# Kernel tuning notes

Measured on AMD Instinct MI355X. Metric: run time of the kernel, lower is better.

The kernel has to match this reference:

```python
import jax, jax.numpy as jnp
import numpy as np

B, IN, H, M = 65536, 128, 256, 32


def setup_inputs() -> dict:
    key = jax.random.key(0)
    ks = jax.random.split(key, 8)
    s_i = 1.0 / np.sqrt(IN + H)
    s_m = 1.0 / np.sqrt(M)
    return {
        "input": jax.random.normal(ks[0], (B, IN), jnp.float32),
        "media": jax.random.normal(ks[1], (B, M), jnp.float32),
        "h_t": jax.random.normal(ks[2], (B, H), jnp.float32),
        "c_t": jax.random.normal(ks[3], (B, H), jnp.float32),
        "Wi": jax.random.normal(ks[4], (H, IN + H), jnp.float32) * s_i,
        "bi": jax.random.normal(ks[5], (H,), jnp.float32) * s_i,
        "Wm": jax.random.normal(ks[6], (H, M), jnp.float32) * s_m,
        "bm": jax.random.normal(ks[7], (H,), jnp.float32) * s_m,
    }


def reference(input, media, h_t, c_t, Wi, bi, Wm, bm):
    # original, so all gates share one pre-activation g.
    combined = jnp.concatenate([input, h_t], axis=1)
    g = combined @ Wi.T + bi                     # [B, H]
    gate = jax.nn.sigmoid(g)                     # i == f == o
    c = c_t * gate + jnp.tanh(g) * gate          # new cell state
    c_r = jnp.tanh(c)
    m = jax.nn.sigmoid(media @ Wm.T + bm)        # media gate [B, H]
    c_f = c - c_r + c_r * m
    h = jnp.tanh(c_f) * gate
    # classification=False -> output is h; returns (output, h, c)
    return (h, h, c)
```

## Files before the change

kernel.cpp:

```cpp
#include <hip/hip_runtime.h>

#define BB  65536
#define INW 128
#define HH  256
#define MM  32
#define KK  (INW + HH)
#define NKC 12

typedef __attribute__((ext_vector_type(8))) short bf16x8;
typedef __attribute__((ext_vector_type(4))) float f32x4;

__device__ __forceinline__ unsigned short f32_to_bf16(float f) {
    union { float f; unsigned u; } v; v.f = f;
    return (unsigned short)((v.u + 0x7fffu + ((v.u >> 16) & 1u)) >> 16);
}

__device__ __forceinline__ bf16x8 cvt8(f32x4 a, f32x4 b) {
    bf16x8 r;
    r[0] = (short)f32_to_bf16(a[0]); r[1] = (short)f32_to_bf16(a[1]);
    r[2] = (short)f32_to_bf16(a[2]); r[3] = (short)f32_to_bf16(a[3]);
    r[4] = (short)f32_to_bf16(b[0]); r[5] = (short)f32_to_bf16(b[1]);
    r[6] = (short)f32_to_bf16(b[2]); r[7] = (short)f32_to_bf16(b[3]);
    return r;
}

__device__ __forceinline__ float rcp_f(float x) { return __builtin_amdgcn_rcpf(x); }
__device__ __forceinline__ float sigmoid_f(float x) { return rcp_f(1.0f + __expf(-x)); }
__device__ __forceinline__ float tanh_f(float x) { return 1.0f - 2.0f * rcp_f(__expf(2.0f * x) + 1.0f); }

__global__ void pack_weights(const float* __restrict__ Wi, const float* __restrict__ Wm,
                             unsigned short* __restrict__ Wi_p, unsigned short* __restrict__ Wm_p) {
    int id = blockIdx.x * 256 + threadIdx.x;
    if (id < 2 * NKC * 8 * 512) {
        int blk = id >> 9;
        int e   = id & 511;
        int lane = e >> 3, j = e & 7;
        int lrow = lane & 15, quad = lane >> 4;
        int h  = blk / (NKC * 8);
        int b  = blk % (NKC * 8);
        int kc = b >> 3;
        int t  = b & 7;
        int n  = h * 128 + t * 16 + lrow;
        int k  = kc * 32 + quad * 8 + j;
        Wi_p[id] = f32_to_bf16(Wi[(size_t)n * KK + k]);
    }
    if (id < 2 * 8 * 512) {
        int blk = id >> 9;
        int e   = id & 511;
        int lane = e >> 3, j = e & 7;
        int lrow = lane & 15, quad = lane >> 4;
        int h = blk >> 3;
        int t = blk & 7;
        int n = h * 128 + t * 16 + lrow;
        Wm_p[id] = f32_to_bf16(Wm[(size_t)n * MM + quad * 8 + j]);
    }
}

__global__ __launch_bounds__(256) void rlstm_main(
    const float* __restrict__ input, const float* __restrict__ media,
    const float* __restrict__ h_t,   const float* __restrict__ c_t,
    const unsigned short* __restrict__ Wi_p, const float* __restrict__ bi,
    const unsigned short* __restrict__ Wm_p, const float* __restrict__ bm,
    float* __restrict__ out)
{
    const int tid  = threadIdx.x;
    const int wave = tid >> 6;
    const int lane = tid & 63;
    const int lrow = lane & 15;
    const int quad = lane >> 4;

    const int m0   = blockIdx.x * 32 + (wave >> 1) * 16;
    const int half = wave & 1;
    const int n0   = half * 128;

    const unsigned short* wip = Wi_p + (size_t)half * (NKC * 8 * 512);
    const unsigned short* wmp = Wm_p + (size_t)half * (8 * 512);

    const int arow = m0 + lrow;

    f32x4 md0 = *(const f32x4*)(media + (size_t)arow * MM + quad * 8);
    f32x4 md1 = *(const f32x4*)(media + (size_t)arow * MM + quad * 8 + 4);

    f32x4 accg[8];
#pragma unroll
    for (int t = 0; t < 8; ++t) accg[t] = (f32x4){0.f, 0.f, 0.f, 0.f};

#pragma unroll
    for (int kc = 0; kc < NKC; ++kc) {
        const float* src = (kc < 4)
            ? (input + (size_t)arow * INW + kc * 32 + quad * 8)
            : (h_t   + (size_t)arow * HH  + (kc - 4) * 32 + quad * 8);
        f32x4 a0 = ((const f32x4*)src)[0];
        f32x4 a1 = ((const f32x4*)src)[1];
        bf16x8 xf = cvt8(a0, a1);
        const unsigned short* wb = wip + (size_t)kc * (8 * 512) + lane * 8;
#pragma unroll
        for (int t = 0; t < 8; ++t) {
            bf16x8 wf = *(const bf16x8*)(wb + t * 512);
            accg[t] = __builtin_amdgcn_mfma_f32_16x16x32_bf16(wf, xf, accg[t], 0, 0, 0);
        }
    }

    bf16x8 mf = cvt8(md0, md1);
    const size_t outH = (size_t)BB * HH;
    const size_t rowbase = (size_t)arow * HH;
#pragma unroll
    for (int t = 0; t < 8; ++t) {
        bf16x8 wmf = *(const bf16x8*)(wmp + t * 512 + lane * 8);
        f32x4 am = __builtin_amdgcn_mfma_f32_16x16x32_bf16(
            wmf, mf, (f32x4){0.f, 0.f, 0.f, 0.f}, 0, 0, 0);

        const int nb = n0 + t * 16 + quad * 4;
        f32x4 bi4 = *(const f32x4*)(bi + nb);
        f32x4 bm4 = *(const f32x4*)(bm + nb);
        const size_t idx = rowbase + nb;
        f32x4 ct4 = *(const f32x4*)(c_t + idx);

        f32x4 h4, c4;
#pragma unroll
        for (int r = 0; r < 4; ++r) {
            float g    = accg[t][r] + bi4[r];
            float mp   = am[r] + bm4[r];
            float gate = sigmoid_f(g);
            float tg   = tanh_f(g);
            float c    = ct4[r] * gate + tg * gate;
            float cr   = tanh_f(c);
            float mg   = sigmoid_f(mp);
            float cf   = c - cr + cr * mg;
            float h    = tanh_f(cf) * gate;
            h4[r] = h; c4[r] = c;
        }
        *(f32x4*)(out + idx)            = h4;
        *(f32x4*)(out + idx + outH)     = h4;
        *(f32x4*)(out + idx + 2 * outH) = c4;
    }
}

extern "C" void kernel_launch(void* const* d_in, const int* in_sizes, int n_in,
                              void* d_out, int out_size, void* d_ws, size_t ws_size,
                              hipStream_t stream) {
    const float* input = (const float*)d_in[0];
    const float* media = (const float*)d_in[1];
    const float* h_t   = (const float*)d_in[2];
    const float* c_t   = (const float*)d_in[3];
    const float* Wi    = (const float*)d_in[4];
    const float* bi    = (const float*)d_in[5];
    const float* Wm    = (const float*)d_in[6];
    const float* bm    = (const float*)d_in[7];
    float* out = (float*)d_out;

    unsigned short* Wi_p = (unsigned short*)d_ws;
    unsigned short* Wm_p = Wi_p + 2 * NKC * 8 * 512;

    hipLaunchKernelGGL(pack_weights, dim3((2 * NKC * 8 * 512 + 255) / 256), dim3(256), 0, stream,
                       Wi, Wm, Wi_p, Wm_p);
    hipLaunchKernelGGL(rlstm_main, dim3(BB / 32), dim3(256), 0, stream,
                       input, media, h_t, c_t, Wi_p, bi, Wm_p, bm, out);
}
```

Before: 394.7 us.

## Double row tile per wave, software-pipeline loads, prefetch c_t, nontemporal stores

Each wave now computes two 16-row tiles, so every weight fragment loaded from global memory feeds two MFMAs instead of one. Activation loads are triple-buffered and weight loads double-buffered across the K loop to hide latency. c_t is prefetched before the epilogue, outputs are written with nontemporal stores, and launch bounds ask for 2 blocks per SM. The cost is much higher register pressure (two accumulator sets plus the buffers), which may lower occupancy or cause spills, and the grid is halved.

```diff
diff --git a/kernel.cpp b/kernel.cpp
--- a/kernel.cpp
+++ b/kernel.cpp
@@ -50,13 +50,35 @@
         int lane = e >> 3, j = e & 7;
         int lrow = lane & 15, quad = lane >> 4;
         int h = blk >> 3;
-        int t = blk & 7;
+        int t = blk & 3 + 0;
+        t = blk & 7;
         int n = h * 128 + t * 16 + lrow;
         Wm_p[id] = f32_to_bf16(Wm[(size_t)n * MM + quad * 8 + j]);
     }
 }
 
-__global__ __launch_bounds__(256) void rlstm_main(
+__device__ __forceinline__ void epilogue4(f32x4 g4, f32x4 am, f32x4 ct4, f32x4 bi4, f32x4 bm4,
+                                          float* __restrict__ p, size_t outH) {
+    f32x4 h4, c4;
+#pragma unroll
+    for (int r = 0; r < 4; ++r) {
+        float g    = g4[r] + bi4[r];
+        float mp   = am[r] + bm4[r];
+        float gate = sigmoid_f(g);
+        float tg   = tanh_f(g);
+        float c    = ct4[r] * gate + tg * gate;
+        float cr   = tanh_f(c);
+        float mg   = sigmoid_f(mp);
+        float cf   = c - cr + cr * mg;
+        float h    = tanh_f(cf) * gate;
+        h4[r] = h; c4[r] = c;
+    }
+    __builtin_nontemporal_store(h4, (f32x4*)p);
+    __builtin_nontemporal_store(h4, (f32x4*)(p + outH));
+    __builtin_nontemporal_store(c4, (f32x4*)(p + 2 * outH));
+}
+
+__global__ __launch_bounds__(256, 2) void rlstm_main(
     const float* __restrict__ input, const float* __restrict__ media,
     const float* __restrict__ h_t,   const float* __restrict__ c_t,
     const unsigned short* __restrict__ Wi_p, const float* __restrict__ bi,
@@ -69,70 +91,92 @@
     const int lrow = lane & 15;
     const int quad = lane >> 4;
 
-    const int m0   = blockIdx.x * 32 + (wave >> 1) * 16;
+    const int m0   = blockIdx.x * 64 + (wave >> 1) * 32;
     const int half = wave & 1;
     const int n0   = half * 128;
 
     const unsigned short* wip = Wi_p + (size_t)half * (NKC * 8 * 512);
     const unsigned short* wmp = Wm_p + (size_t)half * (8 * 512);
 
-    const int arow = m0 + lrow;
-
-    f32x4 md0 = *(const f32x4*)(media + (size_t)arow * MM + quad * 8);
-    f32x4 md1 = *(const f32x4*)(media + (size_t)arow * MM + quad * 8 + 4);
-
-    f32x4 accg[8];
-#pragma unroll
-    for (int t = 0; t < 8; ++t) accg[t] = (f32x4){0.f, 0.f, 0.f, 0.f};
+    const int arowA = m0 + lrow;
+    const int arowB = arowA + 16;
+
+    f32x4 mdA0 = *(const f32x4*)(media + (size_t)arowA * MM + quad * 8);
+    f32x4 mdA1 = *(const f32x4*)(media + (size_t)arowA * MM + quad * 8 + 4);
+    f32x4 mdB0 = *(const f32x4*)(media + (size_t)arowB * MM + quad * 8);
+    f32x4 mdB1 = *(const f32x4*)(media + (size_t)arowB * MM + quad * 8 + 4);
+
+    f32x4 accA[8], accB[8];
+#pragma unroll
+    for (int t = 0; t < 8; ++t) {
+        accA[t] = (f32x4){0.f, 0.f, 0.f, 0.f};
+        accB[t] = (f32x4){0.f, 0.f, 0.f, 0.f};
+    }
+
+    f32x4  abuf[3][4];
+    bf16x8 wbuf[2][8];
+
+#define ACT_SRC(arow, kc) ((kc) < 4 ? (input + (size_t)(arow) * INW + (kc) * 32 + quad * 8) \
+                                    : (h_t   + (size_t)(arow) * HH  + ((kc) - 4) * 32 + quad * 8))
+#define LOAD_ACT(p, kc) { const float* sA_ = ACT_SRC(arowA, kc); const float* sB_ = ACT_SRC(arowB, kc); \
+        abuf[p][0] = ((const f32x4*)sA_)[0]; abuf[p][1] = ((const f32x4*)sA_)[1];                        \
+        abuf[p][2] = ((const f32x4*)sB_)[0]; abuf[p][3] = ((const f32x4*)sB_)[1]; }
+#define LOAD_W(p, kc) { const unsigned short* wb_ = wip + (size_t)(kc) * (8 * 512) + lane * 8;           \
+        _Pragma("unroll") for (int t_ = 0; t_ < 8; ++t_) wbuf[p][t_] = *(const bf16x8*)(wb_ + t_ * 512); }
+
+    LOAD_ACT(0, 0);
+    LOAD_ACT(1, 1);
+    LOAD_W(0, 0);
 
 #pragma unroll
     for (int kc = 0; kc < NKC; ++kc) {
-        const float* src = (kc < 4)
-            ? (input + (size_t)arow * INW + kc * 32 + quad * 8)
-            : (h_t   + (size_t)arow * HH  + (kc - 4) * 32 + quad * 8);
-        f32x4 a0 = ((const f32x4*)src)[0];
-        f32x4 a1 = ((const f32x4*)src)[1];
-        bf16x8 xf = cvt8(a0, a1);
-        const unsigned short* wb = wip + (size_t)kc * (8 * 512) + lane * 8;
+        if (kc + 2 < NKC) { LOAD_ACT((kc + 2) % 3, kc + 2); }
+        if (kc + 1 < NKC) { LOAD_W((kc + 1) & 1, kc + 1); }
+        bf16x8 xa = cvt8(abuf[kc % 3][0], abuf[kc % 3][1]);
+        bf16x8 xb = cvt8(abuf[kc % 3][2], abuf[kc % 3][3]);
 #pragma unroll
         for (int t = 0; t < 8; ++t) {
-            bf16x8 wf = *(const bf16x8*)(wb + t * 512);
-            accg[t] = __builtin_amdgcn_mfma_f32_16x16x32_bf16(wf, xf, accg[t], 0, 0, 0);
+            bf16x8 wf = wbuf[kc & 1][t];
+            accA[t] = __builtin_amdgcn_mfma_f32_16x16x32_bf16(wf, xa, accA[t], 0, 0, 0);
+            accB[t] = __builtin_amdgcn_mfma_f32_16x16x32_bf16(wf, xb, accB[t], 0, 0, 0);
         }
     }
-
-    bf16x8 mf = cvt8(md0, md1);
+#undef ACT_SRC
+#undef LOAD_ACT
+#undef LOAD_W
+
+    const size_t rowbaseA = (size_t)arowA * HH;
+    const size_t rowbaseB = (size_t)arowB * HH;
+
+    bf16x8 wmfr[8];
+#pragma unroll
+    for (int t = 0; t < 8; ++t) wmfr[t] = *(const bf16x8*)(wmp + t * 512 + lane * 8);
+
+    f32x4 cA[8], cB[8];
+#pragma unroll
+    for (int t = 0; t < 8; ++t) {
+        const int nb = n0 + t * 16 + quad * 4;
+        cA[t] = *(const f32x4*)(c_t + rowbaseA + nb);
+        cB[t] = *(const f32x4*)(c_t + rowbaseB + nb);
+    }
+
+    bf16x8 mfA = cvt8(mdA0, mdA1);
+    bf16x8 mfB = cvt8(mdB0, mdB1);
+
     const size_t outH = (size_t)BB * HH;
-    const size_t rowbase = (size_t)arow * HH;
 #pragma unroll
     for (int t = 0; t < 8; ++t) {
-        bf16x8 wmf = *(const bf16x8*)(wmp + t * 512 + lane * 8);
-        f32x4 am = __builtin_amdgcn_mfma_f32_16x16x32_bf16(
-            wmf, mf, (f32x4){0.f, 0.f, 0.f, 0.f}, 0, 0, 0);
+        f32x4 amA = __builtin_amdgcn_mfma_f32_16x16x32_bf16(
+            wmfr[t], mfA, (f32x4){0.f, 0.f, 0.f, 0.f}, 0, 0, 0);
+        f32x4 amB = __builtin_amdgcn_mfma_f32_16x16x32_bf16(
+            wmfr[t], mfB, (f32x4){0.f, 0.f, 0.f, 0.f}, 0, 0, 0);
 
         const int nb = n0 + t * 16 + quad * 4;
         f32x4 bi4 = *(const f32x4*)(bi + nb);
         f32x4 bm4 = *(const f32x4*)(bm + nb);
-        const size_t idx = rowbase + nb;
-        f32x4 ct4 = *(const f32x4*)(c_t + idx);
-
-        f32x4 h4, c4;
-#pragma unroll
-        for (int r = 0; r < 4; ++r) {
-            float g    = accg[t][r] + bi4[r];
-            float mp   = am[r] + bm4[r];
-            float gate = sigmoid_f(g);
-            float tg   = tanh_f(g);
-            float c    = ct4[r] * gate + tg * gate;
-            float cr   = tanh_f(c);
-            float mg   = sigmoid_f(mp);
-            float cf   = c - cr + cr * mg;
-            float h    = tanh_f(cf) * gate;
-            h4[r] = h; c4[r] = c;
-        }
-        *(f32x4*)(out + idx)            = h4;
-        *(f32x4*)(out + idx + outH)     = h4;
-        *(f32x4*)(out + idx + 2 * outH) = c4;
+
+        epilogue4(accA[t], amA, cA[t], bi4, bm4, out + rowbaseA + nb, outH);
+        epilogue4(accB[t], amB, cB[t], bi4, bm4, out + rowbaseB + nb, outH);
     }
 }
 
@@ -154,6 +198,6 @@
 
     hipLaunchKernelGGL(pack_weights, dim3((2 * NKC * 8 * 512 + 255) / 256), dim3(256), 0, stream,
                        Wi, Wm, Wi_p, Wm_p);
-    hipLaunchKernelGGL(rlstm_main, dim3(BB / 32), dim3(256), 0, stream,
+    hipLaunchKernelGGL(rlstm_main, dim3(BB / 64), dim3(256), 0, stream,
                        input, media, h_t, c_t, Wi_p, bi, Wm_p, bm, out);
 }
```

New measurement: 387.9 us. Within noise of the previous version (-1.7%).

## Stage weight quarter in LDS, split N across blocks, prefetch activations, nontemporal stores

Applied to the files above, without the earlier changes.

Each block now handles a 64-column quarter of H for 128 rows: it stages that quarter of the packed bf16 weights and biases in shared memory and loops over two 64-row tiles. Activations for the next tile are prefetched into registers during the current tile's epilogue, using sched barriers to fix the order. Output stores become nontemporal. This trades repeated global weight reads for LDS reuse, but each activation row is now read by four blocks, and the change adds register pressure and an occupancy hint.

```diff
diff --git a/kernel.cpp b/kernel.cpp
--- a/kernel.cpp
+++ b/kernel.cpp
@@ -9,6 +9,8 @@
 
 typedef __attribute__((ext_vector_type(8))) short bf16x8;
 typedef __attribute__((ext_vector_type(4))) float f32x4;
+
+#define SB() __builtin_amdgcn_sched_barrier(0)
 
 __device__ __forceinline__ unsigned short f32_to_bf16(float f) {
     union { float f; unsigned u; } v; v.f = f;
@@ -56,84 +58,127 @@
     }
 }
 
-__global__ __launch_bounds__(256) void rlstm_main(
+__device__ __forceinline__ void epilogue4(f32x4 g4, f32x4 am, f32x4 ct4, f32x4 bi4, f32x4 bm4,
+                                          float* __restrict__ p, size_t outH) {
+    f32x4 h4, c4;
+#pragma unroll
+    for (int r = 0; r < 4; ++r) {
+        float g    = g4[r] + bi4[r];
+        float mp   = am[r] + bm4[r];
+        float gate = sigmoid_f(g);
+        float tg   = tanh_f(g);
+        float c    = ct4[r] * gate + tg * gate;
+        float cr   = tanh_f(c);
+        float mg   = sigmoid_f(mp);
+        float cf   = c - cr + cr * mg;
+        float h    = tanh_f(cf) * gate;
+        h4[r] = h; c4[r] = c;
+    }
+    __builtin_nontemporal_store(h4, (f32x4*)p);
+    __builtin_nontemporal_store(h4, (f32x4*)(p + outH));
+    __builtin_nontemporal_store(c4, (f32x4*)(p + 2 * outH));
+}
+
+__global__ __launch_bounds__(256, 3) void rlstm_main(
     const float* __restrict__ input, const float* __restrict__ media,
     const float* __restrict__ h_t,   const float* __restrict__ c_t,
     const unsigned short* __restrict__ Wi_p, const float* __restrict__ bi,
     const unsigned short* __restrict__ Wm_p, const float* __restrict__ bm,
     float* __restrict__ out)
 {
+    __shared__ unsigned short wiq[NKC * 4 * 512];
+    __shared__ unsigned short wmq[4 * 512];
+    __shared__ float lbi[64], lbm[64];
+
     const int tid  = threadIdx.x;
     const int wave = tid >> 6;
     const int lane = tid & 63;
     const int lrow = lane & 15;
     const int quad = lane >> 4;
 
-    const int m0   = blockIdx.x * 32 + (wave >> 1) * 16;
-    const int half = wave & 1;
-    const int n0   = half * 128;
-
-    const unsigned short* wip = Wi_p + (size_t)half * (NKC * 8 * 512);
-    const unsigned short* wmp = Wm_p + (size_t)half * (8 * 512);
-
-    const int arow = m0 + lrow;
-
-    f32x4 md0 = *(const f32x4*)(media + (size_t)arow * MM + quad * 8);
-    f32x4 md1 = *(const f32x4*)(media + (size_t)arow * MM + quad * 8 + 4);
-
-    f32x4 accg[8];
-#pragma unroll
-    for (int t = 0; t < 8; ++t) accg[t] = (f32x4){0.f, 0.f, 0.f, 0.f};
-
-#pragma unroll
-    for (int kc = 0; kc < NKC; ++kc) {
-        const float* src = (kc < 4)
-            ? (input + (size_t)arow * INW + kc * 32 + quad * 8)
-            : (h_t   + (size_t)arow * HH  + (kc - 4) * 32 + quad * 8);
-        f32x4 a0 = ((const f32x4*)src)[0];
-        f32x4 a1 = ((const f32x4*)src)[1];
-        bf16x8 xf = cvt8(a0, a1);
-        const unsigned short* wb = wip + (size_t)kc * (8 * 512) + lane * 8;
-#pragma unroll
-        for (int t = 0; t < 8; ++t) {
-            bf16x8 wf = *(const bf16x8*)(wb + t * 512);
-            accg[t] = __builtin_amdgcn_mfma_f32_16x16x32_bf16(wf, xf, accg[t], 0, 0, 0);
+    const int q      = blockIdx.x & 3;
+    const int half   = q >> 1;
+    const int thalf  = q & 1;
+    const int n0q    = q * 64;
+    const int rowblk = blockIdx.x >> 2;
+
+    const int arow0 = rowblk * 128 + wave * 16 + lrow;
+
+    f32x4 act[24];
+#define ACT_PTR(arow, kc) ((kc) < 4 ? (input + (size_t)(arow) * INW + (kc) * 32 + quad * 8) \
+                                    : (h_t   + (size_t)(arow) * HH  + ((kc) - 4) * 32 + quad * 8))
+#define LOAD_ACTS(arow) { _Pragma("unroll") for (int kc_ = 0; kc_ < NKC; ++kc_) {            \
+        const float* s_ = ACT_PTR(arow, kc_);                                                \
+        act[2 * kc_]     = ((const f32x4*)s_)[0];                                            \
+        act[2 * kc_ + 1] = ((const f32x4*)s_)[1]; } }
+
+    LOAD_ACTS(arow0);
+    SB();
+
+#pragma unroll
+    for (int r = 0; r < 12; ++r) {
+        int le  = (r * 256 + tid) * 8;
+        int kc  = le >> 11;
+        int rem = le & 2047;
+        bf16x8 v = *(const bf16x8*)(Wi_p + (size_t)(half * NKC + kc) * 4096 + thalf * 2048 + rem);
+        *(bf16x8*)(wiq + le) = v;
+    }
+    {
+        int le = tid * 8;
+        bf16x8 v = *(const bf16x8*)(Wm_p + (size_t)half * 4096 + thalf * 2048 + le);
+        *(bf16x8*)(wmq + le) = v;
+    }
+    if (tid < 64)        lbi[tid]      = bi[n0q + tid];
+    else if (tid < 128)  lbm[tid - 64] = bm[n0q + (tid - 64)];
+    __syncthreads();
+
+    const size_t outH = (size_t)BB * HH;
+
+#pragma unroll
+    for (int tl = 0; tl < 2; ++tl) {
+        const int arow = arow0 + tl * 64;
+        const size_t rowbase = (size_t)arow * HH + n0q;
+
+        f32x4 ct[4];
+        SB();
+#pragma unroll
+        for (int t = 0; t < 4; ++t)
+            ct[t] = *(const f32x4*)(c_t + rowbase + t * 16 + quad * 4);
+        f32x4 md0 = *(const f32x4*)(media + (size_t)arow * MM + quad * 8);
+        f32x4 md1 = *(const f32x4*)(media + (size_t)arow * MM + quad * 8 + 4);
+        SB();
+
+        f32x4 acc[4];
+#pragma unroll
+        for (int t = 0; t < 4; ++t) acc[t] = (f32x4){0.f, 0.f, 0.f, 0.f};
+#pragma unroll
+        for (int kc = 0; kc < NKC; ++kc) {
+            bf16x8 xa = cvt8(act[2 * kc], act[2 * kc + 1]);
+#pragma unroll
+            for (int t = 0; t < 4; ++t) {
+                bf16x8 wf = *(const bf16x8*)(wiq + kc * 2048 + t * 512 + lane * 8);
+                acc[t] = __builtin_amdgcn_mfma_f32_16x16x32_bf16(wf, xa, acc[t], 0, 0, 0);
+            }
         }
-    }
-
-    bf16x8 mf = cvt8(md0, md1);
-    const size_t outH = (size_t)BB * HH;
-    const size_t rowbase = (size_t)arow * HH;
-#pragma unroll
-    for (int t = 0; t < 8; ++t) {
-        bf16x8 wmf = *(const bf16x8*)(wmp + t * 512 + lane * 8);
-        f32x4 am = __builtin_amdgcn_mfma_f32_16x16x32_bf16(
-            wmf, mf, (f32x4){0.f, 0.f, 0.f, 0.f}, 0, 0, 0);
-
-        const int nb = n0 + t * 16 + quad * 4;
-        f32x4 bi4 = *(const f32x4*)(bi + nb);
-        f32x4 bm4 = *(const f32x4*)(bm + nb);
-        const size_t idx = rowbase + nb;
-        f32x4 ct4 = *(const f32x4*)(c_t + idx);
-
-        f32x4 h4, c4;
-#pragma unroll
-        for (int r = 0; r < 4; ++r) {
-            float g    = accg[t][r] + bi4[r];
-            float mp   = am[r] + bm4[r];
-            float gate = sigmoid_f(g);
-            float tg   = tanh_f(g);
-            float c    = ct4[r] * gate + tg * gate;
-            float cr   = tanh_f(c);
-            float mg   = sigmoid_f(mp);
-            float cf   = c - cr + cr * mg;
-            float h    = tanh_f(cf) * gate;
-            h4[r] = h; c4[r] = c;
+        SB();
+        if (tl == 0) { LOAD_ACTS(arow0 + 64); }
+        SB();
+
+        bf16x8 mf = cvt8(md0, md1);
+#pragma unroll
+        for (int t = 0; t < 4; ++t) {
+            bf16x8 wmf = *(const bf16x8*)(wmq + t * 512 + lane * 8);
+            f32x4 am = __builtin_amdgcn_mfma_f32_16x16x32_bf16(
+                wmf, mf, (f32x4){0.f, 0.f, 0.f, 0.f}, 0, 0, 0);
+            const int nb = t * 16 + quad * 4;
+            f32x4 bi4 = *(const f32x4*)(lbi + nb);
+            f32x4 bm4 = *(const f32x4*)(lbm + nb);
+            epilogue4(acc[t], am, ct[t], bi4, bm4, out + rowbase + nb, outH);
         }
-        *(f32x4*)(out + idx)            = h4;
-        *(f32x4*)(out + idx + outH)     = h4;
-        *(f32x4*)(out + idx + 2 * outH) = c4;
-    }
+        SB();
+    }
+#undef ACT_PTR
+#undef LOAD_ACTS
 }
 
 extern "C" void kernel_launch(void* const* d_in, const int* in_sizes, int n_in,
@@ -154,6 +199,6 @@
 
     hipLaunchKernelGGL(pack_weights, dim3((2 * NKC * 8 * 512 + 255) / 256), dim3(256), 0, stream,
                        Wi, Wm, Wi_p, Wm_p);
-    hipLaunchKernelGGL(rlstm_main, dim3(BB / 32), dim3(256), 0, stream,
+    hipLaunchKernelGGL(rlstm_main, dim3(512 * 4), dim3(256), 0, stream,
                        input, media, h_t, c_t, Wi_p, bi, Wm_p, bm, out);
 }
```

After: 369.9 us. 1.07x faster.
